# Kernel tuning notes

Hardware: AMD Instinct MI355X
Metric: run time of the kernel (lower is better)

Reference implementation:

```python
import jax, jax.numpy as jnp
import numpy as np

N_NODES = 50000
N_EDGES = 200000
N_GRAPHS = 1024
D = 24          # node feature dim (fixed by Set2Set(24))
E_FEAT = 8
E_HID = 128


def setup_inputs() -> dict:
    key = jax.random.key(0)
    ks = jax.random.split(key, 20)
    s = 0.1  # weight scale for numerical sanity
    inp = {
        "x": jax.random.normal(ks[0], (N_NODES, D), jnp.float32),
        "edge_attr": jax.random.normal(ks[1], (N_EDGES, E_FEAT), jnp.float32),
        # edge-network MLP: E_FEAT -> E_HID -> D*D
        "w_e1": jax.random.normal(ks[2], (E_FEAT, E_HID), jnp.float32) * s,
        "b_e1": jnp.zeros((E_HID,), jnp.float32),
        "w_e2": jax.random.normal(ks[3], (E_HID, D * D), jnp.float32) * s,
        "b_e2": jnp.zeros((D * D,), jnp.float32),
        # NNConv root weight + bias
        "root": jax.random.normal(ks[4], (D, D), jnp.float32) * s,
        "bias_conv": jnp.zeros((D,), jnp.float32),
        # Set2Set LSTM (input 2D=48, hidden D=24), torch gate order i,f,g,o
        "w_ih": jax.random.normal(ks[5], (4 * D, 2 * D), jnp.float32) * s,
        "w_hh": jax.random.normal(ks[6], (4 * D, D), jnp.float32) * s,
        "b_ih": jnp.zeros((4 * D,), jnp.float32),
        "b_hh": jnp.zeros((4 * D,), jnp.float32),
        # heads
        "w_fc2": jax.random.normal(ks[7], (2 * D, 8), jnp.float32) * s,
        "b_fc2": jnp.zeros((8,), jnp.float32),
        "w_fc3": jax.random.normal(ks[8], (8, 2), jnp.float32) * s,
        "b_fc3": jnp.zeros((2,), jnp.float32),
        "edge_index": jax.random.randint(ks[9], (2, N_EDGES), 0, N_NODES, jnp.int64),
        "batch": jnp.sort(jax.random.randint(ks[10], (N_NODES,), 0, N_GRAPHS, jnp.int64)),
    }
    return inp


def _nnconv(x, edge_attr, edge_index, w_e1, b_e1, w_e2, b_e2, root, bias_conv):
    src, dst = edge_index[0], edge_index[1]
    h = jax.nn.relu(edge_attr @ w_e1 + b_e1)
    w = (h @ w_e2 + b_e2).reshape(-1, D, D)          # [E, D_in, D_out]
    msg = jnp.einsum('ei,eio->eo', x[src], w)         # gather + per-edge matvec
    s = jax.ops.segment_sum(msg, dst, num_segments=N_NODES)
    cnt = jax.ops.segment_sum(jnp.ones((msg.shape[0],), msg.dtype), dst, num_segments=N_NODES)
    agg = s / jnp.maximum(cnt, 1.0)[:, None]          # scatter-mean
    return agg + x @ root + bias_conv


def _set2set(x, batch, w_ih, w_hh, b_ih, b_hh):
    B = N_GRAPHS
    q_star = jnp.zeros((B, 2 * D), x.dtype)
    h = jnp.zeros((B, D), x.dtype)
    c = jnp.zeros((B, D), x.dtype)
    for _ in range(3):  # processing_steps=3 (fixed small loop)
        gates = q_star @ w_ih.T + b_ih + h @ w_hh.T + b_hh
        i, f, g, o = jnp.split(gates, 4, axis=-1)
        c = jax.nn.sigmoid(f) * c + jax.nn.sigmoid(i) * jnp.tanh(g)
        h = jax.nn.sigmoid(o) * jnp.tanh(c)
        q = h                                         # [B, D]
        e = jnp.sum(x * q[batch], axis=-1)            # [N]
        e_max = jax.ops.segment_max(e, batch, num_segments=B)
        e_max = jnp.where(jnp.isfinite(e_max), e_max, 0.0)
        ex = jnp.exp(e - e_max[batch])
        denom = jax.ops.segment_sum(ex, batch, num_segments=B)
        a = ex / jnp.maximum(denom, 1e-16)[batch]     # per-graph softmax
        r = jax.ops.segment_sum(a[:, None] * x, batch, num_segments=B)
        q_star = jnp.concatenate([q, r], axis=-1)
    return q_star


def reference(x, edge_attr, w_e1, b_e1, w_e2, b_e2, root, bias_conv,
              w_ih, w_hh, b_ih, b_hh, w_fc2, b_fc2, w_fc3, b_fc3,
              edge_index, batch):
    x = _nnconv(x, edge_attr, edge_index, w_e1, b_e1, w_e2, b_e2, root, bias_conv)
    x = jax.nn.relu(x)
    x = _nnconv(x, edge_attr, edge_index, w_e1, b_e1, w_e2, b_e2, root, bias_conv)
    q_star = _set2set(x, batch, w_ih, w_hh, b_ih, b_hh)
    out = jax.nn.relu(q_star @ w_fc2 + b_fc2)
    return out @ w_fc3 + b_fc3                        # [B, 2]
```

## Files before the change

### kernel.cpp

```cpp
#include <hip/hip_runtime.h>
#include <math.h>

#define N_NODES 50000
#define N_EDGES 200000
#define N_GRAPHS 1024
#define DIM 24
#define EF 8
#define EH 128
#define DD 576
#define HSTR 136

typedef __attribute__((ext_vector_type(8))) _Float16 f16x8;
typedef __attribute__((ext_vector_type(4))) _Float16 f16x4;
typedef __attribute__((ext_vector_type(2))) _Float16 f16x2;
typedef __attribute__((ext_vector_type(4))) float float4e;
typedef _Float16 f16;

static __device__ __forceinline__ float sigm(float x) { return 1.0f / (1.0f + expf(-x)); }

__global__ __launch_bounds__(256) void prep_kernel(
    const int* __restrict__ dst, int* __restrict__ deg,
    const float* __restrict__ w2, const float* __restrict__ b2,
    f16* __restrict__ Bz)
{
    const int b = blockIdx.x, t = threadIdx.x;
    if (b < 782) {
        int i = b * 256 + t;
        if (i < N_EDGES) atomicAdd(&deg[dst[i]], 1);
        return;
    }
    int idx = (b - 782) * 256 + t;
    if (idx >= 97 * 2 * 64 * 8) return;
    int kk = idx & 7, lane = (idx >> 3) & 63, nt = (idx >> 9) & 1, p = idx >> 10;
    int q = lane >> 4, l16 = lane & 15, n = nt * 16 + l16;
    float v = 0.0f;
    if (p < 96) {
        int si = p / 24, i = p % 24;
        int k = si * 32 + q * 8 + kk;
        if (n < 24) v = w2[(size_t)k * DD + i * 24 + n];
    } else {
        int i2 = q * 8 + kk;
        if (i2 < 24 && n < 24) v = b2[i2 * 24 + n];
    }
    Bz[idx] = (f16)v;
}

__global__ __launch_bounds__(256, 4) void conv_kernel(
    const float* __restrict__ x, const float* __restrict__ ea,
    const float* __restrict__ w1, const float* __restrict__ b1,
    const f16* __restrict__ Bz,
    const int* __restrict__ src, const int* __restrict__ dst,
    float* __restrict__ agg)
{
    __shared__ f16 hs[128 * HSTR];

    const int t  = threadIdx.x;
    const int e0 = blockIdx.x * 128;

    const int lane = t & 63;
    const int wave = t >> 6;
    const int l16  = lane & 15;
    const int quad = lane >> 4;
    const int ebase = e0 + wave * 32;

    f16x2 xa[12], xb[12];
    {
        int ega = ebase + l16;      if (ega >= N_EDGES) ega = N_EDGES - 1;
        int egb = ebase + 16 + l16; if (egb >= N_EDGES) egb = N_EDGES - 1;
        const float* xra = x + (size_t)src[ega] * DIM;
        const float* xrb = x + (size_t)src[egb] * DIM;
        #pragma unroll
        for (int j4 = 0; j4 < 6; ++j4) {
            float4 va = *(const float4*)(xra + j4 * 4);
            float4 vb = *(const float4*)(xrb + j4 * 4);
            xa[j4 * 2]     = (f16x2){(f16)va.x, (f16)va.y};
            xa[j4 * 2 + 1] = (f16x2){(f16)va.z, (f16)va.w};
            xb[j4 * 2]     = (f16x2){(f16)vb.x, (f16)vb.y};
            xb[j4 * 2 + 1] = (f16x2){(f16)vb.z, (f16)vb.w};
        }
    }

    {
        const int s5 = t & 31;
        const int eb = (t >> 5) * 16;
        float wv[EF][4];
        #pragma unroll
        for (int j = 0; j < EF; ++j) {
            float4 v = *(const float4*)(w1 + j * EH + s5 * 4);
            wv[j][0] = v.x; wv[j][1] = v.y; wv[j][2] = v.z; wv[j][3] = v.w;
        }
        float4 bv = *(const float4*)(b1 + s5 * 4);
        const float bvv[4] = {bv.x, bv.y, bv.z, bv.w};
        #pragma unroll
        for (int e = 0; e < 16; ++e) {
            int eg = e0 + eb + e; if (eg >= N_EDGES) eg = N_EDGES - 1;
            const float* ear = ea + (size_t)eg * EF;
            float4 a0 = *(const float4*)ear;
            float4 a1 = *(const float4*)(ear + 4);
            const float av[EF] = {a0.x, a0.y, a0.z, a0.w, a1.x, a1.y, a1.z, a1.w};
            float r[4] = {bvv[0], bvv[1], bvv[2], bvv[3]};
            #pragma unroll
            for (int j = 0; j < EF; ++j)
                #pragma unroll
                for (int c = 0; c < 4; ++c)
                    r[c] = fmaf(av[j], wv[j][c], r[c]);
            f16x4 hq = { (f16)fmaxf(r[0], 0.0f), (f16)fmaxf(r[1], 0.0f),
                         (f16)fmaxf(r[2], 0.0f), (f16)fmaxf(r[3], 0.0f) };
            *(f16x4*)&hs[(eb + e) * HSTR + s5 * 4] = hq;
        }
    }

    const f16x8* bz = (const f16x8*)Bz + lane;
    f16x8 pb0[4], pb1[4];
    #pragma unroll
    for (int s = 0; s < 4; ++s) { pb0[s] = bz[s * 128]; pb1[s] = bz[s * 128 + 64]; }

    __syncthreads();

    float4e a00 = {0.f,0.f,0.f,0.f}, a01 = {0.f,0.f,0.f,0.f};
    float4e a10 = {0.f,0.f,0.f,0.f}, a11 = {0.f,0.f,0.f,0.f};

    #pragma unroll
    for (int si = 0; si < 4; ++si) {
        union { f16x8 v; f16x2 p[4]; } h0u, h1u;
        h0u.v = *(const f16x8*)&hs[(wave * 32 + l16) * HSTR + si * 32 + quad * 8];
        h1u.v = *(const f16x8*)&hs[(wave * 32 + 16 + l16) * HSTR + si * 32 + quad * 8];
        #pragma unroll
        for (int i = 0; i < 24; ++i) {
            const int p = si * 24 + i;
            f16x8 b0 = pb0[p & 3], b1v = pb1[p & 3];
            if (p + 4 <= 96) {
                pb0[p & 3] = bz[(p + 4) * 128];
                pb1[p & 3] = bz[(p + 4) * 128 + 64];
            }
            f16 xea = (i & 1) ? xa[i >> 1][1] : xa[i >> 1][0];
            f16 xeb = (i & 1) ? xb[i >> 1][1] : xb[i >> 1][0];
            f16x2 xa2 = {xea, xea}, xb2 = {xeb, xeb};
            union { f16x8 v; f16x2 p[4]; } a0u, a1u;
            #pragma unroll
            for (int j = 0; j < 4; ++j) {
                a0u.p[j] = h0u.p[j] * xa2;
                a1u.p[j] = h1u.p[j] * xb2;
            }
            a00 = __builtin_amdgcn_mfma_f32_16x16x32_f16(a0u.v, b0,  a00, 0, 0, 0);
            a10 = __builtin_amdgcn_mfma_f32_16x16x32_f16(a1u.v, b0,  a10, 0, 0, 0);
            a01 = __builtin_amdgcn_mfma_f32_16x16x32_f16(a0u.v, b1v, a01, 0, 0, 0);
            a11 = __builtin_amdgcn_mfma_f32_16x16x32_f16(a1u.v, b1v, a11, 0, 0, 0);
            if ((p % 12) == 11) __builtin_amdgcn_s_barrier();
        }
    }

    {
        union { f16x8 v; f16x2 p[4]; } a0u, a1u;
        f16x2 z2 = {(f16)0.f, (f16)0.f};
        if (quad == 0)      { a0u.p[0]=xa[0]; a0u.p[1]=xa[1]; a0u.p[2]=xa[2];  a0u.p[3]=xa[3];
                              a1u.p[0]=xb[0]; a1u.p[1]=xb[1]; a1u.p[2]=xb[2];  a1u.p[3]=xb[3];  }
        else if (quad == 1) { a0u.p[0]=xa[4]; a0u.p[1]=xa[5]; a0u.p[2]=xa[6];  a0u.p[3]=xa[7];
                              a1u.p[0]=xb[4]; a1u.p[1]=xb[5]; a1u.p[2]=xb[6];  a1u.p[3]=xb[7];  }
        else if (quad == 2) { a0u.p[0]=xa[8]; a0u.p[1]=xa[9]; a0u.p[2]=xa[10]; a0u.p[3]=xa[11];
                              a1u.p[0]=xb[8]; a1u.p[1]=xb[9]; a1u.p[2]=xb[10]; a1u.p[3]=xb[11]; }
        else                { a0u.p[0]=z2; a0u.p[1]=z2; a0u.p[2]=z2; a0u.p[3]=z2;
                              a1u.p[0]=z2; a1u.p[1]=z2; a1u.p[2]=z2; a1u.p[3]=z2; }
        a00 = __builtin_amdgcn_mfma_f32_16x16x32_f16(a0u.v, pb0[0], a00, 0, 0, 0);
        a10 = __builtin_amdgcn_mfma_f32_16x16x32_f16(a1u.v, pb0[0], a10, 0, 0, 0);
        a01 = __builtin_amdgcn_mfma_f32_16x16x32_f16(a0u.v, pb1[0], a01, 0, 0, 0);
        a11 = __builtin_amdgcn_mfma_f32_16x16x32_f16(a1u.v, pb1[0], a11, 0, 0, 0);
    }

    #pragma unroll
    for (int r = 0; r < 4; ++r) {
        int er = ebase + quad * 4 + r;
        if (er < N_EDGES) {
            int d = dst[er];
            atomicAdd(&agg[(size_t)d * DIM + l16], a00[r]);
            if (l16 < 8) atomicAdd(&agg[(size_t)d * DIM + 16 + l16], a01[r]);
        }
        int er2 = ebase + 16 + quad * 4 + r;
        if (er2 < N_EDGES) {
            int d = dst[er2];
            atomicAdd(&agg[(size_t)d * DIM + l16], a10[r]);
            if (l16 < 8) atomicAdd(&agg[(size_t)d * DIM + 16 + l16], a11[r]);
        }
    }
}

__global__ void combine_kernel(
    const float* __restrict__ x_in, float* __restrict__ agg,
    const int* __restrict__ deg, const float* __restrict__ root,
    const float* __restrict__ bias, float* __restrict__ x_out,
    int do_relu, int zero_agg)
{
    int t = blockIdx.x * blockDim.x + threadIdx.x;
    if (t >= N_NODES * DIM) return;
    int v = t / DIM, o = t % DIM;
    int dg = deg[v];
    float d = dg > 0 ? (float)dg : 1.0f;
    float a = agg[t] / d + bias[o];
    if (zero_agg) agg[t] = 0.0f;
    const float* xr = x_in + (size_t)v * DIM;
    #pragma unroll
    for (int i = 0; i < DIM; ++i) a = fmaf(xr[i], root[i * DIM + o], a);
    x_out[t] = do_relu ? fmaxf(a, 0.0f) : a;
}

__global__ __launch_bounds__(64) void s2s_kernel(
    const float* __restrict__ x, const int* __restrict__ batch,
    const float* __restrict__ w_ih, const float* __restrict__ w_hh,
    const float* __restrict__ b_ih, const float* __restrict__ b_hh,
    const float* __restrict__ w_fc2, const float* __restrict__ b_fc2,
    const float* __restrict__ w_fc3, const float* __restrict__ b_fc3,
    float* __restrict__ out)
{
    const int g = blockIdx.x;
    const int t = threadIdx.x;
    __shared__ float qs[48];
    __shared__ float hh[24], cc[24], gates[96], zl[8];
    __shared__ int s_lo, s_hi;

    if (t == 0) {
        int lo = 0, hi = N_NODES;
        while (lo < hi) { int m = (lo + hi) >> 1; if (batch[m] < g) lo = m + 1; else hi = m; }
        s_lo = lo;
        int lo2 = lo; hi = N_NODES;
        while (lo2 < hi) { int m = (lo2 + hi) >> 1; if (batch[m] <= g) lo2 = m + 1; else hi = m; }
        s_hi = lo2;
    }
    if (t < 48) qs[t] = 0.0f;
    if (t < 24) { hh[t] = 0.0f; cc[t] = 0.0f; }
    __syncthreads();
    const int lo = s_lo, hi = s_hi;

    for (int it = 0; it < 3; ++it) {
        for (int rr = t; rr < 96; rr += 64) {
            float a = b_ih[rr] + b_hh[rr];
            const float* wi = w_ih + (size_t)rr * 48;
            const float* wh = w_hh + (size_t)rr * 24;
            #pragma unroll
            for (int j4 = 0; j4 < 12; ++j4) {
                float4 w = *(const float4*)(wi + j4 * 4);
                a = fmaf(qs[j4*4+0], w.x, a); a = fmaf(qs[j4*4+1], w.y, a);
                a = fmaf(qs[j4*4+2], w.z, a); a = fmaf(qs[j4*4+3], w.w, a);
            }
            #pragma unroll
            for (int j4 = 0; j4 < 6; ++j4) {
                float4 w = *(const float4*)(wh + j4 * 4);
                a = fmaf(hh[j4*4+0], w.x, a); a = fmaf(hh[j4*4+1], w.y, a);
                a = fmaf(hh[j4*4+2], w.z, a); a = fmaf(hh[j4*4+3], w.w, a);
            }
            gates[rr] = a;
        }
        __syncthreads();
        if (t < 24) {
            float c = sigm(gates[24 + t]) * cc[t] + sigm(gates[t]) * tanhf(gates[48 + t]);
            cc[t] = c;
            float h = sigm(gates[72 + t]) * tanhf(c);
            hh[t] = h;
            qs[t] = h;
        }
        __syncthreads();

        float m_l = -INFINITY, s_l = 0.0f;
        float r_l[24];
        #pragma unroll
        for (int d = 0; d < 24; ++d) r_l[d] = 0.0f;
        for (int n = lo + t; n < hi; n += 64) {
            float xv[24];
            #pragma unroll
            for (int j = 0; j < 6; ++j)
                *(float4*)&xv[j * 4] = ((const float4*)(x + (size_t)n * DIM))[j];
            float e = 0.0f;
            #pragma unroll
            for (int d = 0; d < 24; ++d) e = fmaf(xv[d], qs[d], e);
            if (e > m_l) {
                float sc = expf(m_l - e);
                #pragma unroll
                for (int d = 0; d < 24; ++d) r_l[d] *= sc;
                s_l *= sc;
                m_l = e;
            }
            float w = expf(e - m_l);
            s_l += w;
            #pragma unroll
            for (int d = 0; d < 24; ++d) r_l[d] = fmaf(w, xv[d], r_l[d]);
        }
        float m = m_l;
        #pragma unroll
        for (int off = 32; off; off >>= 1) m = fmaxf(m, __shfl_xor(m, off));
        float fac = (m_l == -INFINITY) ? 0.0f : expf(m_l - m);
        float s = s_l * fac;
        #pragma unroll
        for (int off = 32; off; off >>= 1) s += __shfl_xor(s, off);
        float denom = fmaxf(s, 1e-16f);
        #pragma unroll
        for (int d = 0; d < 24; ++d) {
            float rv = r_l[d] * fac;
            #pragma unroll
            for (int off = 32; off; off >>= 1) rv += __shfl_xor(rv, off);
            if (t == d) qs[24 + d] = rv / denom;
        }
        __syncthreads();
    }

    if (t < 8) {
        float a = b_fc2[t];
        #pragma unroll
        for (int j = 0; j < 48; ++j) a = fmaf(qs[j], w_fc2[j * 8 + t], a);
        zl[t] = fmaxf(a, 0.0f);
    }
    __syncthreads();
    if (t < 2) {
        float a = b_fc3[t];
        #pragma unroll
        for (int k = 0; k < 8; ++k) a = fmaf(zl[k], w_fc3[k * 2 + t], a);
        out[(size_t)g * 2 + t] = a;
    }
}

extern "C" void kernel_launch(void* const* d_in, const int* in_sizes, int n_in,
                              void* d_out, int out_size, void* d_ws, size_t ws_size,
                              hipStream_t stream) {
    const float* x      = (const float*)d_in[0];
    const float* ea     = (const float*)d_in[1];
    const float* w_e1   = (const float*)d_in[2];
    const float* b_e1   = (const float*)d_in[3];
    const float* w_e2   = (const float*)d_in[4];
    const float* b_e2   = (const float*)d_in[5];
    const float* root   = (const float*)d_in[6];
    const float* bias_c = (const float*)d_in[7];
    const float* w_ih   = (const float*)d_in[8];
    const float* w_hh   = (const float*)d_in[9];
    const float* b_ih   = (const float*)d_in[10];
    const float* b_hh   = (const float*)d_in[11];
    const float* w_fc2  = (const float*)d_in[12];
    const float* b_fc2  = (const float*)d_in[13];
    const float* w_fc3  = (const float*)d_in[14];
    const float* b_fc3  = (const float*)d_in[15];
    const int*   eidx   = (const int*)d_in[16];
    const int*   batch  = (const int*)d_in[17];
    const int* esrc = eidx;
    const int* edst = eidx + N_EDGES;
    float* out = (float*)d_out;

    char* ws = (char*)d_ws;
    float* agg   = (float*)(ws);
    int*   deg   = (int*)  (ws + 4800000);
    float* x1    = (float*)(ws + 5789824);
    float* x2    = (float*)(ws + 10589824);
    f16*   Bz    = (f16*)  (ws + 15389824);

    hipMemsetAsync(ws, 0, 5000000, stream);

    prep_kernel<<<782 + 388, 256, 0, stream>>>(edst, deg, w_e2, b_e2, Bz);

    conv_kernel<<<(N_EDGES + 127) / 128, 256, 0, stream>>>(x, ea, w_e1, b_e1, Bz, esrc, edst, agg);
    combine_kernel<<<(N_NODES * DIM + 255) / 256, 256, 0, stream>>>(x, agg, deg, root, bias_c, x1, 1, 1);

    conv_kernel<<<(N_EDGES + 127) / 128, 256, 0, stream>>>(x1, ea, w_e1, b_e1, Bz, esrc, edst, agg);
    combine_kernel<<<(N_NODES * DIM + 255) / 256, 256, 0, stream>>>(x1, agg, deg, root, bias_c, x2, 0, 0);

    s2s_kernel<<<N_GRAPHS, 64, 0, stream>>>(x2, batch, w_ih, w_hh, b_ih, b_hh,
                                            w_fc2, b_fc2, w_fc3, b_fc3, out);
}
```

Measured before the change: 291.1 us.

## Enlarge conv blocks to 512 threads and vectorize combine with transposed root

The edge-conv kernel now processes 256 edges per block with 512 threads and a doubled shared hidden buffer, halving the block count. The combine kernel is restructured so each thread handles six outputs of one node, loading the node row as float4s and using a transposed root matrix prepared in prep_kernel. This aims to cut redundant x row loads and scalar root reads in combine. The larger conv block uses about 68KB of LDS per block, which may lower occupancy.

```diff
diff --git a/kernel.cpp b/kernel.cpp
--- a/kernel.cpp
+++ b/kernel.cpp
@@ -21,7 +21,8 @@
 __global__ __launch_bounds__(256) void prep_kernel(
     const int* __restrict__ dst, int* __restrict__ deg,
     const float* __restrict__ w2, const float* __restrict__ b2,
-    f16* __restrict__ Bz)
+    const float* __restrict__ root,
+    f16* __restrict__ Bz, float* __restrict__ rootT)
 {
     const int b = blockIdx.x, t = threadIdx.x;
     if (b < 782) {
@@ -29,33 +30,41 @@
         if (i < N_EDGES) atomicAdd(&deg[dst[i]], 1);
         return;
     }
-    int idx = (b - 782) * 256 + t;
-    if (idx >= 97 * 2 * 64 * 8) return;
-    int kk = idx & 7, lane = (idx >> 3) & 63, nt = (idx >> 9) & 1, p = idx >> 10;
-    int q = lane >> 4, l16 = lane & 15, n = nt * 16 + l16;
-    float v = 0.0f;
-    if (p < 96) {
-        int si = p / 24, i = p % 24;
-        int k = si * 32 + q * 8 + kk;
-        if (n < 24) v = w2[(size_t)k * DD + i * 24 + n];
-    } else {
-        int i2 = q * 8 + kk;
-        if (i2 < 24 && n < 24) v = b2[i2 * 24 + n];
-    }
-    Bz[idx] = (f16)v;
-}
-
-__global__ __launch_bounds__(256, 4) void conv_kernel(
+    if (b < 1170) {
+        int idx = (b - 782) * 256 + t;
+        if (idx >= 97 * 2 * 64 * 8) return;
+        int kk = idx & 7, lane = (idx >> 3) & 63, nt = (idx >> 9) & 1, p = idx >> 10;
+        int q = lane >> 4, l16 = lane & 15, n = nt * 16 + l16;
+        float v = 0.0f;
+        if (p < 96) {
+            int si = p / 24, i = p % 24;
+            int k = si * 32 + q * 8 + kk;
+            if (n < 24) v = w2[(size_t)k * DD + i * 24 + n];
+        } else {
+            int i2 = q * 8 + kk;
+            if (i2 < 24 && n < 24) v = b2[i2 * 24 + n];
+        }
+        Bz[idx] = (f16)v;
+        return;
+    }
+    int idx = (b - 1170) * 256 + t;
+    if (idx < DD) {
+        int i = idx / 24, o = idx % 24;
+        rootT[o * 24 + i] = root[idx];
+    }
+}
+
+__global__ __launch_bounds__(512, 4) void conv_kernel(
     const float* __restrict__ x, const float* __restrict__ ea,
     const float* __restrict__ w1, const float* __restrict__ b1,
     const f16* __restrict__ Bz,
     const int* __restrict__ src, const int* __restrict__ dst,
     float* __restrict__ agg)
 {
-    __shared__ f16 hs[128 * HSTR];
+    __shared__ f16 hs[256 * HSTR];
 
     const int t  = threadIdx.x;
-    const int e0 = blockIdx.x * 128;
+    const int e0 = blockIdx.x * 256;
 
     const int lane = t & 63;
     const int wave = t >> 6;
@@ -184,23 +193,47 @@
     }
 }
 
-__global__ void combine_kernel(
+__global__ __launch_bounds__(256) void combine_kernel(
     const float* __restrict__ x_in, float* __restrict__ agg,
-    const int* __restrict__ deg, const float* __restrict__ root,
+    const int* __restrict__ deg, const float* __restrict__ rootT,
     const float* __restrict__ bias, float* __restrict__ x_out,
     int do_relu, int zero_agg)
 {
-    int t = blockIdx.x * blockDim.x + threadIdx.x;
-    if (t >= N_NODES * DIM) return;
-    int v = t / DIM, o = t % DIM;
+    int gid = blockIdx.x * 256 + threadIdx.x;
+    int v = gid >> 2, q = gid & 3;
+    if (v >= N_NODES) return;
+    const int o0 = q * 6;
+
+    float xv[24];
+    const float4* xr = (const float4*)(x_in + (size_t)v * DIM);
+    #pragma unroll
+    for (int j = 0; j < 6; ++j) *(float4*)&xv[j * 4] = xr[j];
+
     int dg = deg[v];
-    float d = dg > 0 ? (float)dg : 1.0f;
-    float a = agg[t] / d + bias[o];
-    if (zero_agg) agg[t] = 0.0f;
-    const float* xr = x_in + (size_t)v * DIM;
-    #pragma unroll
-    for (int i = 0; i < DIM; ++i) a = fmaf(xr[i], root[i * DIM + o], a);
-    x_out[t] = do_relu ? fmaxf(a, 0.0f) : a;
+    float dinv = 1.0f / (dg > 0 ? (float)dg : 1.0f);
+    float* aggr = agg + (size_t)v * DIM + o0;
+
+    float r[6];
+    #pragma unroll
+    for (int u = 0; u < 6; ++u) {
+        int o = o0 + u;
+        float a = aggr[u] * dinv + bias[o];
+        const float4* rt = (const float4*)(rootT + o * 24);
+        #pragma unroll
+        for (int j = 0; j < 6; ++j) {
+            float4 w = rt[j];
+            a = fmaf(xv[j*4+0], w.x, a); a = fmaf(xv[j*4+1], w.y, a);
+            a = fmaf(xv[j*4+2], w.z, a); a = fmaf(xv[j*4+3], w.w, a);
+        }
+        r[u] = do_relu ? fmaxf(a, 0.0f) : a;
+    }
+    if (zero_agg) {
+        #pragma unroll
+        for (int u = 0; u < 6; ++u) aggr[u] = 0.0f;
+    }
+    float* xo = x_out + (size_t)v * DIM + o0;
+    #pragma unroll
+    for (int u = 0; u < 6; ++u) xo[u] = r[u];
 }
 
 __global__ __launch_bounds__(64) void s2s_kernel(
@@ -347,16 +380,17 @@
     float* x1    = (float*)(ws + 5789824);
     float* x2    = (float*)(ws + 10589824);
     f16*   Bz    = (f16*)  (ws + 15389824);
+    float* rootT = (float*)(ws + 15588480);
 
     hipMemsetAsync(ws, 0, 5000000, stream);
 
-    prep_kernel<<<782 + 388, 256, 0, stream>>>(edst, deg, w_e2, b_e2, Bz);
-
-    conv_kernel<<<(N_EDGES + 127) / 128, 256, 0, stream>>>(x, ea, w_e1, b_e1, Bz, esrc, edst, agg);
-    combine_kernel<<<(N_NODES * DIM + 255) / 256, 256, 0, stream>>>(x, agg, deg, root, bias_c, x1, 1, 1);
-
-    conv_kernel<<<(N_EDGES + 127) / 128, 256, 0, stream>>>(x1, ea, w_e1, b_e1, Bz, esrc, edst, agg);
-    combine_kernel<<<(N_NODES * DIM + 255) / 256, 256, 0, stream>>>(x1, agg, deg, root, bias_c, x2, 0, 0);
+    prep_kernel<<<1173, 256, 0, stream>>>(edst, deg, w_e2, b_e2, root, Bz, rootT);
+
+    conv_kernel<<<(N_EDGES + 255) / 256, 512, 0, stream>>>(x, ea, w_e1, b_e1, Bz, esrc, edst, agg);
+    combine_kernel<<<(N_NODES * 4 + 255) / 256, 256, 0, stream>>>(x, agg, deg, rootT, bias_c, x1, 1, 1);
+
+    conv_kernel<<<(N_EDGES + 255) / 256, 512, 0, stream>>>(x1, ea, w_e1, b_e1, Bz, esrc, edst, agg);
+    combine_kernel<<<(N_NODES * 4 + 255) / 256, 256, 0, stream>>>(x1, agg, deg, rootT, bias_c, x2, 0, 0);
 
     s2s_kernel<<<N_GRAPHS, 64, 0, stream>>>(x2, batch, w_ih, w_hh, b_ih, b_hh,
                                             w_fc2, b_fc2, w_fc3, b_fc3, out);
```

Measured after the change: 323.0 us. +11.0%, slower.
